# Kernel tuning notes

Measured on AMD Instinct MI355X. Metric: run time of the kernel, lower is better.

The kernel has to match this reference:

```python
import jax, jax.numpy as jnp
import numpy as np
from jax import lax

T = 1_000_000  # time steps
K = 64         # hidden states


def setup_inputs() -> dict:
    key = jax.random.key(0)
    k1, k2, k3, k4 = jax.random.split(key, 4)
    return {
        "y": jax.random.normal(k1, (T,), dtype=jnp.float32),
        "transition_logits": jax.random.normal(k2, (K, K), dtype=jnp.float32),
        "mu": jax.random.normal(k3, (K,), dtype=jnp.float32),
        "log_sigma": jax.random.normal(k4, (K,), dtype=jnp.float32) * 0.1,
    }


def _stationary_distribution(P):
    # Solve pi^T P = pi^T with sum(pi) = 1 via a linear system (differentiable).
    k = P.shape[0]
    A = jnp.transpose(P) - jnp.eye(k, dtype=P.dtype)
    A = A.at[-1, :].set(jnp.ones((k,), dtype=P.dtype))
    b = jnp.zeros((k,), dtype=P.dtype).at[-1].set(1.0)
    return jnp.linalg.solve(A, b)


def reference(y, transition_logits, mu, log_sigma):
    # Row-stochastic transition matrix [K, K]
    P = jax.nn.softmax(transition_logits, axis=-1)
    sigma = jnp.exp(log_sigma)  # [K]
    # Univariate Gaussian emission densities g[t, k] = N(y_t; mu_k, sigma_k^2)
    z = (y[:, None] - mu[None, :]) / sigma[None, :]           # [T, K]
    inv_norm = 1.0 / (sigma * jnp.sqrt(2.0 * jnp.pi))         # [K]
    g = jnp.exp(-0.5 * z * z) * inv_norm[None, :]             # [T, K]

    ut0 = _stationary_distribution(P)        # initial (predicted) distribution
    g0 = g[0]
    ft0 = jnp.sum(ut0 * g0)                  # normalizer at t=0
    utt0 = ut0 * g0 / ft0                    # filtered distribution at t=0

    def step(utt, gt):
        ut = utt @ P                         # predict: [K]
        num = ut * gt
        ft = jnp.sum(num)
        utt_new = num / ft                   # update (normalize)
        return utt_new, (ut, ft, utt_new)

    _, (Ut, ft_rest, Utt) = lax.scan(step, utt0, g[1:])

    ut = jnp.concatenate([ut0[None, :], Ut], axis=0)        # [T, K] predicted
    u_norm = jnp.concatenate([utt0[None, :], Utt], axis=0)  # [T, K] filtered
    ft = jnp.concatenate([ft0[None], ft_rest], axis=0)      # [T] normalizers
    return ut, u_norm, ft
```

## Files before the change

kernel.cpp:

```cpp
#include <hip/hip_runtime.h>

#define K 64
#define S_CHUNK 128
#define W_BURN 96
#define BATCH 16

typedef __attribute__((ext_vector_type(4))) _Float16 half4;
typedef __attribute__((ext_vector_type(4))) float f32x4;

__device__ __forceinline__ float waveReduceSum(float v) {
#pragma unroll
    for (int off = 32; off > 0; off >>= 1) v += __shfl_xor(v, off, 64);
    return v;
}

#define WS_P     0
#define WS_PI    4096
#define WS_UTT0  4160
#define WS_ISG   4224
#define WS_NNU   4288
#define WS_L2N   4352

__global__ __launch_bounds__(64) void hmm_setup(
    const float* __restrict__ y, const float* __restrict__ logits,
    const float* __restrict__ mu, const float* __restrict__ log_sigma,
    float* __restrict__ out, float* __restrict__ ws, int T)
{
    __shared__ float P[K][K];
    __shared__ float pib[K];
    const int k = threadIdx.x;

    float row[K]; float m = -3.4e38f;
#pragma unroll
    for (int i = 0; i < K; ++i) { row[i] = logits[k*K + i]; m = fmaxf(m, row[i]); }
    float s = 0.f;
#pragma unroll
    for (int i = 0; i < K; ++i) { row[i] = __expf(row[i] - m); s += row[i]; }
    float inv = 1.0f / s;
#pragma unroll
    for (int i = 0; i < K; ++i) { float p = row[i]*inv; P[k][i] = p; ws[WS_P + k*K + i] = p; }
    __syncthreads();

    pib[k] = 1.0f/64.0f;
    __syncthreads();
    for (int it = 0; it < 64; ++it) {
        float acc = 0.f;
#pragma unroll
        for (int j = 0; j < K; ++j) acc += pib[j]*P[j][k];
        float tot = waveReduceSum(acc);
        acc /= tot;
        __syncthreads();
        pib[k] = acc;
        __syncthreads();
    }
    float pi_k = pib[k];

    float mu_k = mu[k];
    float isg = __expf(-log_sigma[k]);
    float inorm = isg * 0.39894228040143267f;

    ws[WS_PI  + k] = pi_k;
    ws[WS_ISG + k] = isg;
    ws[WS_NNU + k] = -mu_k * isg;
    ws[WS_L2N + k] = __log2f(inorm);

    float y0 = y[0];
    float z = (y0 - mu_k) * isg;
    float g0 = __expf(-0.5f*z*z) * inorm;
    float num = pi_k * g0;
    float ft0 = waveReduceSum(num);
    float utt0 = num / ft0;
    ws[WS_UTT0 + k] = utt0;

    out[k] = pi_k;
    out[(size_t)T*K + k] = utt0;
    if (k == 0) out[(size_t)2*T*K] = ft0;
}

__global__ __launch_bounds__(64) void hmm_scan(
    const float* __restrict__ y, const float* __restrict__ ws,
    float* __restrict__ out, int T)
{
    __shared__ float lut[16][260];
    __shared__ float lun[16][260];
    __shared__ float lft[16][4];
    const int lane = threadIdx.x;
    const int c = lane & 15;
    const int q = lane >> 4;
    const int cg = blockIdx.x * BATCH + c;
    const int t0 = cg * S_CHUNK;
    (void)t0;

    float* const ou_ = out + (size_t)T * K;
    float* const of_ = out + (size_t)2 * T * K;

    half4 a[4][4];
#pragma unroll
    for (int nb = 0; nb < 4; ++nb)
#pragma unroll
        for (int kb = 0; kb < 4; ++kb)
#pragma unroll
            for (int j = 0; j < 4; ++j)
                a[nb][kb][j] = (_Float16)ws[WS_P + (16*kb + 4*q + j)*K + 16*nb + c];

    f32x4 isg_[4], nnu_[4], l2n_[4];
#pragma unroll
    for (int nb = 0; nb < 4; ++nb)
#pragma unroll
        for (int r = 0; r < 4; ++r) {
            int s = 16*nb + 4*q + r;
            isg_[nb][r] = ws[WS_ISG + s];
            nnu_[nb][r] = ws[WS_NNU + s];
            l2n_[nb][r] = ws[WS_L2N + s];
        }

    half4 bfr[4], u0h[4];
#pragma unroll
    for (int kb = 0; kb < 4; ++kb)
#pragma unroll
        for (int j = 0; j < 4; ++j) {
            int s = 16*kb + 4*q + j;
            bfr[kb][j] = (_Float16)ws[WS_PI + s];
            u0h[kb][j] = (_Float16)ws[WS_UTT0 + s];
        }

    int tcur = t0 - W_BURN;
    int ib = min(max(tcur, 0), T - 4);
    f32x4 yv = *(const f32x4*)(y + ib);

#define STEP(OUTP, YCUR, II) do {                                              \
    f32x4 accA_[4] = {{0.f,0.f,0.f,0.f},{0.f,0.f,0.f,0.f},                     \
                      {0.f,0.f,0.f,0.f},{0.f,0.f,0.f,0.f}};                    \
    f32x4 accB_[4] = {{0.f,0.f,0.f,0.f},{0.f,0.f,0.f,0.f},                     \
                      {0.f,0.f,0.f,0.f},{0.f,0.f,0.f,0.f}};                    \
    _Pragma("unroll")                                                          \
    for (int nb_ = 0; nb_ < 4; ++nb_)                                          \
        accA_[nb_] = __builtin_amdgcn_mfma_f32_16x16x16f16(a[nb_][0], bfr[0], accA_[nb_], 0,0,0); \
    _Pragma("unroll")                                                          \
    for (int nb_ = 0; nb_ < 4; ++nb_)                                          \
        accB_[nb_] = __builtin_amdgcn_mfma_f32_16x16x16f16(a[nb_][2], bfr[2], accB_[nb_], 0,0,0); \
    _Pragma("unroll")                                                          \
    for (int nb_ = 0; nb_ < 4; ++nb_)                                          \
        accA_[nb_] = __builtin_amdgcn_mfma_f32_16x16x16f16(a[nb_][1], bfr[1], accA_[nb_], 0,0,0); \
    _Pragma("unroll")                                                          \
    for (int nb_ = 0; nb_ < 4; ++nb_)                                          \
        accB_[nb_] = __builtin_amdgcn_mfma_f32_16x16x16f16(a[nb_][3], bfr[3], accB_[nb_], 0,0,0); \
    f32x4 acc_[4];                                                             \
    _Pragma("unroll")                                                          \
    for (int nb_ = 0; nb_ < 4; ++nb_) acc_[nb_] = accA_[nb_] + accB_[nb_];     \
    if (OUTP) {                                                                \
        _Pragma("unroll")                                                      \
        for (int nb_ = 0; nb_ < 4; ++nb_)                                      \
            *(f32x4*)&lut[c][(II)*64 + 16*nb_ + 4*q] = acc_[nb_];              \
    }                                                                          \
    f32x4 nrm[4]; float st = 0.f;                                              \
    _Pragma("unroll")                                                          \
    for (int nb_ = 0; nb_ < 4; ++nb_) {                                        \
        _Pragma("unroll")                                                      \
        for (int r_ = 0; r_ < 4; ++r_) {                                       \
            float z  = fmaf(YCUR, isg_[nb_][r_], nnu_[nb_][r_]);               \
            float ag = fmaf(z*z, -0.72134752f, l2n_[nb_][r_]);                 \
            float g  = __builtin_amdgcn_exp2f(ag);                             \
            nrm[nb_][r_] = acc_[nb_][r_] * g;                                  \
            st += nrm[nb_][r_];                                                \
        }                                                                      \
    }                                                                          \
    st += __shfl_xor(st, 16, 64);                                              \
    st += __shfl_xor(st, 32, 64);                                              \
    const float rs = __builtin_amdgcn_rcpf(st);                                \
    _Pragma("unroll")                                                          \
    for (int nb_ = 0; nb_ < 4; ++nb_) nrm[nb_] *= rs;                          \
    if (OUTP) {                                                                \
        _Pragma("unroll")                                                      \
        for (int nb_ = 0; nb_ < 4; ++nb_)                                      \
            *(f32x4*)&lun[c][(II)*64 + 16*nb_ + 4*q] = nrm[nb_];               \
        if (lane < 16) lft[lane][(II)] = st;                                   \
    }                                                                          \
    _Pragma("unroll")                                                          \
    for (int kb_ = 0; kb_ < 4; ++kb_) {                                        \
        auto lo_ = __builtin_amdgcn_cvt_pkrtz(nrm[kb_][0], nrm[kb_][1]);       \
        auto hi_ = __builtin_amdgcn_cvt_pkrtz(nrm[kb_][2], nrm[kb_][3]);       \
        bfr[kb_][0] = (_Float16)lo_[0]; bfr[kb_][1] = (_Float16)lo_[1];        \
        bfr[kb_][2] = (_Float16)hi_[0]; bfr[kb_][3] = (_Float16)hi_[1];        \
    }                                                                          \
    ++tcur;                                                                    \
} while (0)

#define FLUSH(TB) do {                                                         \
    const int rowb_ = blockIdx.x * (BATCH * S_CHUNK) + (TB);                   \
    const bool sp_ = (blockIdx.x == 0) && ((TB) == 0);                         \
    _Pragma("unroll")                                                          \
    for (int j_ = 0; j_ < 16; ++j_) {                                          \
        int row_ = rowb_ + j_ * S_CHUNK;                                       \
        if (row_ < T) {                                                        \
            f32x4 vu_ = *(const f32x4*)&lut[j_][lane * 4];                     \
            f32x4 vn_ = *(const f32x4*)&lun[j_][lane * 4];                     \
            size_t off_ = (size_t)row_ * K + lane * 4;                         \
            if (!(sp_ && (j_ == 0) && (lane < 16))) {                          \
                *(f32x4*)(out + off_) = vu_;                                   \
                *(f32x4*)(ou_ + off_) = vn_;                                   \
            }                                                                  \
        }                                                                      \
    }                                                                          \
    {                                                                          \
        int jf_ = lane >> 2, if_ = lane & 3;                                   \
        int rowf_ = rowb_ + jf_ * S_CHUNK;                                     \
        float fv_ = lft[jf_][if_];                                             \
        if ((rowf_ < T) && !(sp_ && (lane == 0))) of_[rowf_ + if_] = fv_;      \
    }                                                                          \
} while (0)

#pragma unroll 1
    for (int gi = 0; gi < W_BURN/4; ++gi) {
        int ibn = min(max(tcur + 4, 0), T - 4);
        f32x4 yn = *(const f32x4*)(y + ibn);
        STEP(0, yv[0], 0); STEP(0, yv[1], 1); STEP(0, yv[2], 2); STEP(0, yv[3], 3);
        yv = yn;
    }
    {
        int ibn = min(max(tcur + 4, 0), T - 4);
        f32x4 yn = *(const f32x4*)(y + ibn);
        STEP(1, yv[0], 0);
        if (cg == 0) { bfr[0]=u0h[0]; bfr[1]=u0h[1]; bfr[2]=u0h[2]; bfr[3]=u0h[3]; }
        STEP(1, yv[1], 1); STEP(1, yv[2], 2); STEP(1, yv[3], 3);
        FLUSH(0);
        yv = yn;
    }
#pragma unroll 1
    for (int gi = 1; gi < S_CHUNK/4; ++gi) {
        int ibn = min(max(tcur + 4, 0), T - 4);
        f32x4 yn = *(const f32x4*)(y + ibn);
        STEP(1, yv[0], 0); STEP(1, yv[1], 1); STEP(1, yv[2], 2); STEP(1, yv[3], 3);
        FLUSH(gi * 4);
        yv = yn;
    }
#undef STEP
#undef FLUSH
}

extern "C" void kernel_launch(void* const* d_in, const int* in_sizes, int n_in,
                              void* d_out, int out_size, void* d_ws, size_t ws_size,
                              hipStream_t stream) {
    const float* y      = (const float*)d_in[0];
    const float* logits = (const float*)d_in[1];
    const float* mu     = (const float*)d_in[2];
    const float* lsig   = (const float*)d_in[3];
    float* out = (float*)d_out;
    float* ws  = (float*)d_ws;
    const int T = in_sizes[0];

    hmm_setup<<<1, 64, 0, stream>>>(y, logits, mu, lsig, out, ws, T);

    const int nch  = (T + S_CHUNK - 1) / S_CHUNK;
    const int nblk = (nch + BATCH - 1) / BATCH;
    hmm_scan<<<nblk, 64, 0, stream>>>(y, ws, out, T);
}
```

Baseline: 206.3 us.

## Stage outputs as packed fp16 in LDS, flush every 8 steps with nontemporal stores

The staging buffers for predicted and filtered distributions now hold packed fp16 pairs instead of fp32. This halves LDS footprint and LDS write traffic per step. Flushes to global memory happen every 8 steps instead of 4 and use nontemporal stores to avoid cache pollution. The burn-in warmup is shortened from 96 to 80 steps to cut redundant recomputation. Output values lose precision by passing through fp16, and the shorter burn-in may leave chunk-boundary states less converged.

Measured after the change: 223.0 us. 1.08x slower.

```diff
diff --git a/kernel.cpp b/kernel.cpp
--- a/kernel.cpp
+++ b/kernel.cpp
@@ -2,9 +2,10 @@
 
 #define K 64
 #define S_CHUNK 128
-#define W_BURN 96
+#define W_BURN 80
 #define BATCH 16
 
+typedef __attribute__((ext_vector_type(2))) __fp16 fp16x2;
 typedef __attribute__((ext_vector_type(4))) _Float16 half4;
 typedef __attribute__((ext_vector_type(4))) float f32x4;
 
@@ -12,6 +13,17 @@
 #pragma unroll
     for (int off = 32; off > 0; off >>= 1) v += __shfl_xor(v, off, 64);
     return v;
+}
+
+__device__ __forceinline__ unsigned pkh(float a, float b) {
+    auto t = __builtin_amdgcn_cvt_pkrtz(a, b);
+    return __builtin_bit_cast(unsigned, t);
+}
+
+__device__ __forceinline__ f32x4 unpk2(unsigned x, unsigned y) {
+    fp16x2 a = __builtin_bit_cast(fp16x2, x);
+    fp16x2 b = __builtin_bit_cast(fp16x2, y);
+    return f32x4{(float)a[0], (float)a[1], (float)b[0], (float)b[1]};
 }
 
 #define WS_P     0
@@ -81,15 +93,14 @@
     const float* __restrict__ y, const float* __restrict__ ws,
     float* __restrict__ out, int T)
 {
-    __shared__ float lut[16][260];
-    __shared__ float lun[16][260];
-    __shared__ float lft[16][4];
+    __shared__ __align__(16) unsigned lutp[16][256];
+    __shared__ __align__(16) unsigned lunp[16][256];
+    __shared__ float lft[16][8];
     const int lane = threadIdx.x;
     const int c = lane & 15;
     const int q = lane >> 4;
     const int cg = blockIdx.x * BATCH + c;
     const int t0 = cg * S_CHUNK;
-    (void)t0;
 
     float* const ou_ = out + (size_t)T * K;
     float* const of_ = out + (size_t)2 * T * K;
@@ -150,8 +161,11 @@
     for (int nb_ = 0; nb_ < 4; ++nb_) acc_[nb_] = accA_[nb_] + accB_[nb_];     \
     if (OUTP) {                                                                \
         _Pragma("unroll")                                                      \
-        for (int nb_ = 0; nb_ < 4; ++nb_)                                      \
-            *(f32x4*)&lut[c][(II)*64 + 16*nb_ + 4*q] = acc_[nb_];              \
+        for (int nb_ = 0; nb_ < 4; ++nb_) {                                    \
+            unsigned alo_ = pkh(acc_[nb_][0], acc_[nb_][1]);                   \
+            unsigned ahi_ = pkh(acc_[nb_][2], acc_[nb_][3]);                   \
+            *(uint2*)&lutp[c][(II)*32 + 8*nb_ + 2*q] = make_uint2(alo_, ahi_); \
+        }                                                                      \
     }                                                                          \
     f32x4 nrm[4]; float st = 0.f;                                              \
     _Pragma("unroll")                                                          \
@@ -170,16 +184,16 @@
     const float rs = __builtin_amdgcn_rcpf(st);                                \
     _Pragma("unroll")                                                          \
     for (int nb_ = 0; nb_ < 4; ++nb_) nrm[nb_] *= rs;                          \
-    if (OUTP) {                                                                \
-        _Pragma("unroll")                                                      \
-        for (int nb_ = 0; nb_ < 4; ++nb_)                                      \
-            *(f32x4*)&lun[c][(II)*64 + 16*nb_ + 4*q] = nrm[nb_];               \
-        if (lane < 16) lft[lane][(II)] = st;                                   \
-    }                                                                          \
+    if (OUTP) { if (lane < 16) lft[lane][(II)] = st; }                         \
     _Pragma("unroll")                                                          \
     for (int kb_ = 0; kb_ < 4; ++kb_) {                                        \
         auto lo_ = __builtin_amdgcn_cvt_pkrtz(nrm[kb_][0], nrm[kb_][1]);       \
         auto hi_ = __builtin_amdgcn_cvt_pkrtz(nrm[kb_][2], nrm[kb_][3]);       \
+        if (OUTP) {                                                            \
+            *(uint2*)&lunp[c][(II)*32 + 8*kb_ + 2*q] =                         \
+                make_uint2(__builtin_bit_cast(unsigned, lo_),                  \
+                           __builtin_bit_cast(unsigned, hi_));                 \
+        }                                                                      \
         bfr[kb_][0] = (_Float16)lo_[0]; bfr[kb_][1] = (_Float16)lo_[1];        \
         bfr[kb_][2] = (_Float16)hi_[0]; bfr[kb_][3] = (_Float16)hi_[1];        \
     }                                                                          \
@@ -191,22 +205,39 @@
     const bool sp_ = (blockIdx.x == 0) && ((TB) == 0);                         \
     _Pragma("unroll")                                                          \
     for (int j_ = 0; j_ < 16; ++j_) {                                          \
-        int row_ = rowb_ + j_ * S_CHUNK;                                       \
-        if (row_ < T) {                                                        \
-            f32x4 vu_ = *(const f32x4*)&lut[j_][lane * 4];                     \
-            f32x4 vn_ = *(const f32x4*)&lun[j_][lane * 4];                     \
-            size_t off_ = (size_t)row_ * K + lane * 4;                         \
-            if (!(sp_ && (j_ == 0) && (lane < 16))) {                          \
-                *(f32x4*)(out + off_) = vu_;                                   \
-                *(f32x4*)(ou_ + off_) = vn_;                                   \
+        _Pragma("unroll")                                                      \
+        for (int u_ = 0; u_ < 2; ++u_) {                                       \
+            int rb_ = rowb_ + j_ * S_CHUNK + u_ * 4;                           \
+            if (rb_ < T) {                                                     \
+                uint2 w_ = *(const uint2*)&lutp[j_][u_*128 + lane*2];          \
+                f32x4 v_ = unpk2(w_.x, w_.y);                                  \
+                if (!(sp_ && (j_ == 0) && (u_ == 0) && (lane < 16)))           \
+                    __builtin_nontemporal_store(v_, (f32x4*)(out +             \
+                        (size_t)(rowb_ + j_*S_CHUNK)*K + u_*256 + lane*4));    \
             }                                                                  \
         }                                                                      \
     }                                                                          \
-    {                                                                          \
-        int jf_ = lane >> 2, if_ = lane & 3;                                   \
-        int rowf_ = rowb_ + jf_ * S_CHUNK;                                     \
-        float fv_ = lft[jf_][if_];                                             \
-        if ((rowf_ < T) && !(sp_ && (lane == 0))) of_[rowf_ + if_] = fv_;      \
+    _Pragma("unroll")                                                          \
+    for (int j_ = 0; j_ < 16; ++j_) {                                          \
+        _Pragma("unroll")                                                      \
+        for (int u_ = 0; u_ < 2; ++u_) {                                       \
+            int rb_ = rowb_ + j_ * S_CHUNK + u_ * 4;                           \
+            if (rb_ < T) {                                                     \
+                uint2 w_ = *(const uint2*)&lunp[j_][u_*128 + lane*2];          \
+                f32x4 v_ = unpk2(w_.x, w_.y);                                  \
+                if (!(sp_ && (j_ == 0) && (u_ == 0) && (lane < 16)))           \
+                    __builtin_nontemporal_store(v_, (f32x4*)(ou_ +             \
+                        (size_t)(rowb_ + j_*S_CHUNK)*K + u_*256 + lane*4));    \
+            }                                                                  \
+        }                                                                      \
+    }                                                                          \
+    _Pragma("unroll")                                                          \
+    for (int uu_ = 0; uu_ < 2; ++uu_) {                                        \
+        int idx_ = uu_ * 64 + lane;                                            \
+        int jf_ = idx_ >> 3, ii_ = idx_ & 7;                                   \
+        int tf_ = rowb_ + jf_ * S_CHUNK + ii_;                                 \
+        float fv_ = lft[jf_][ii_];                                             \
+        if ((tf_ < T) && !(sp_ && (idx_ == 0))) of_[tf_] = fv_;                \
     }                                                                          \
 } while (0)
 
@@ -223,15 +254,21 @@
         STEP(1, yv[0], 0);
         if (cg == 0) { bfr[0]=u0h[0]; bfr[1]=u0h[1]; bfr[2]=u0h[2]; bfr[3]=u0h[3]; }
         STEP(1, yv[1], 1); STEP(1, yv[2], 2); STEP(1, yv[3], 3);
+        yv = yn;
+        ibn = min(max(tcur + 4, 0), T - 4);
+        yn = *(const f32x4*)(y + ibn);
+        STEP(1, yv[0], 4); STEP(1, yv[1], 5); STEP(1, yv[2], 6); STEP(1, yv[3], 7);
         FLUSH(0);
         yv = yn;
     }
 #pragma unroll 1
-    for (int gi = 1; gi < S_CHUNK/4; ++gi) {
+    for (int gi = 2; gi < S_CHUNK/4; ++gi) {
         int ibn = min(max(tcur + 4, 0), T - 4);
         f32x4 yn = *(const f32x4*)(y + ibn);
-        STEP(1, yv[0], 0); STEP(1, yv[1], 1); STEP(1, yv[2], 2); STEP(1, yv[3], 3);
-        FLUSH(gi * 4);
+        const int i0 = (gi & 1) * 4;
+        STEP(1, yv[0], i0 + 0); STEP(1, yv[1], i0 + 1);
+        STEP(1, yv[2], i0 + 2); STEP(1, yv[3], i0 + 3);
+        if (gi & 1) FLUSH((gi - 1) * 4);
         yv = yn;
     }
 #undef STEP
```
